# Optimization experiments

Hardware: AMD Instinct MI355X
Metric: run time of the kernel (lower is better)

The kernel has to match this reference:

```python
import jax, jax.numpy as jnp
import numpy as np

IN_FEATURES = 4096
OUT_FEATURES = 4096
NUM_TILES = 4


def setup_inputs() -> dict:
    key = jax.random.key(0)
    k1, k2, k3, k4 = jax.random.split(key, 4)
    x = jax.random.normal(k1, (4096, IN_FEATURES), dtype=jnp.float32)
    gate = jax.random.randint(k2, (4096, NUM_TILES), 0, 2, dtype=jnp.int32)
    # weights initialized ternary via sign(kaiming) in the module; emulate with sign(randn)
    weight = jnp.sign(jax.random.normal(k3, (OUT_FEATURES, IN_FEATURES), dtype=jnp.float32))
    scales = jax.random.uniform(k4, (OUT_FEATURES,), dtype=jnp.float32, minval=0.5, maxval=1.5)
    return {"x": x, "gate": gate, "weight": weight, "scales": scales}


def reference(x, gate, weight, scales):
    # TriX inference semantics: ternary (sign) weights, per-output scale,
    # per-sample tile gating of output columns.
    w = jnp.sign(weight)                       # [O, I] ternary
    out = jnp.matmul(x, w.T) * scales          # [B, O]
    tile_size = OUT_FEATURES // NUM_TILES
    # expand gate [B, T] -> mask over output features [B, O]
    mask = jnp.repeat(gate.astype(out.dtype), tile_size, axis=1)
    return out * mask
```

## Files before the change

kernel.cpp:

```cpp
#include <hip/hip_runtime.h>
#include <stdint.h>

#define M_DIM 4096
#define N_DIM 4096
#define K_DIM 4096
#define BM 128
#define BN 128
#define BKB 128

typedef __attribute__((ext_vector_type(4))) int     int4v;
typedef __attribute__((ext_vector_type(4))) float   f32x4;
typedef __attribute__((ext_vector_type(8))) uint8_t u8x8;

#define XSCALE (127.0f / 4.25f)
#define XDEQ   (4.25f / 127.0f)

__device__ __forceinline__ int8_t q8(float v) {
    float c = fminf(fmaxf(v * XSCALE, -127.0f), 127.0f);
    return (int8_t)(int)__builtin_rintf(c);
}
__device__ __forceinline__ int8_t s8(float v) {
    return (int8_t)((v > 0.0f) - (v < 0.0f));
}

__global__ __launch_bounds__(256) void cvt_i8_kernel(const float* __restrict__ x,
                                                     const float* __restrict__ w,
                                                     int8_t* __restrict__ xq,
                                                     int8_t* __restrict__ wq,
                                                     int n8each) {
    int idx = blockIdx.x * 256 + threadIdx.x;
    u8x8 o;
    if (idx < n8each) {
        const f32x4* s = (const f32x4*)x;
        f32x4 a = s[idx * 2], b = s[idx * 2 + 1];
        o[0] = (uint8_t)q8(a[0]); o[1] = (uint8_t)q8(a[1]);
        o[2] = (uint8_t)q8(a[2]); o[3] = (uint8_t)q8(a[3]);
        o[4] = (uint8_t)q8(b[0]); o[5] = (uint8_t)q8(b[1]);
        o[6] = (uint8_t)q8(b[2]); o[7] = (uint8_t)q8(b[3]);
        *(u8x8*)(xq + (size_t)idx * 8) = o;
    } else {
        int i = idx - n8each;
        const f32x4* s = (const f32x4*)w;
        f32x4 a = s[i * 2], b = s[i * 2 + 1];
        o[0] = (uint8_t)s8(a[0]); o[1] = (uint8_t)s8(a[1]);
        o[2] = (uint8_t)s8(a[2]); o[3] = (uint8_t)s8(a[3]);
        o[4] = (uint8_t)s8(b[0]); o[5] = (uint8_t)s8(b[1]);
        o[6] = (uint8_t)s8(b[2]); o[7] = (uint8_t)s8(b[3]);
        *(u8x8*)(wq + (size_t)i * 8) = o;
    }
}

__device__ __forceinline__ void gload_lds16(const int8_t* g, int8_t* l) {
    __builtin_amdgcn_global_load_lds(
        (__attribute__((address_space(1))) void*)(g),
        (__attribute__((address_space(3))) void*)(l),
        16, 0, 0);
}

__global__ __launch_bounds__(256, 2) void trix_gemm(
    const int8_t* __restrict__ A,
    const int8_t* __restrict__ B,
    const int* __restrict__ gate,
    const float* __restrict__ scales,
    float* __restrict__ out)
{
    __shared__ __align__(16) int8_t As[BM * BKB];
    __shared__ __align__(16) int8_t Bs[BN * BKB];

    const int tid  = threadIdx.x;
    const int lane = tid & 63;
    const int wave = tid >> 6;
    const int wm   = wave >> 1;
    const int wn   = wave & 1;
    const int quad = lane >> 4;
    const int ln16 = lane & 15;

    const int m0 = blockIdx.y * BM;
    const int n0 = blockIdx.x * BN;

    const int srow   = lane >> 3;
    const int gchunk = (lane & 7) ^ srow;
    const int8_t* a_src[4];
    const int8_t* b_src[4];
    int8_t* a_dst[4];
    int8_t* b_dst[4];
#pragma unroll
    for (int j = 0; j < 4; ++j) {
        int cidx = j * 4 + wave;
        a_src[j] = A + (size_t)(m0 + cidx * 8 + srow) * K_DIM + gchunk * 16;
        b_src[j] = B + (size_t)(n0 + cidx * 8 + srow) * K_DIM + gchunk * 16;
        a_dst[j] = As + cidx * 1024;
        b_dst[j] = Bs + cidx * 1024;
    }

    const int8_t* a_rd[4][2];
    const int8_t* b_rd[4][2];
#pragma unroll
    for (int i = 0; i < 4; ++i) {
        int arow = wm * 64 + i * 16 + ln16;
        int brow = wn * 64 + i * 16 + ln16;
#pragma unroll
        for (int kk = 0; kk < 2; ++kk) {
            int ch = quad + 4 * kk;
            a_rd[i][kk] = As + arow * 128 + ((ch ^ (arow & 7)) * 16);
            b_rd[i][kk] = Bs + brow * 128 + ((ch ^ (brow & 7)) * 16);
        }
    }

    int4v acc[4][4];
#pragma unroll
    for (int i = 0; i < 4; ++i)
#pragma unroll
        for (int j = 0; j < 4; ++j)
            acc[i][j] = (int4v){0, 0, 0, 0};

    for (int kt = 0; kt < K_DIM; kt += BKB) {
#pragma unroll
        for (int j = 0; j < 4; ++j) {
            gload_lds16(a_src[j], a_dst[j]);
            gload_lds16(b_src[j], b_dst[j]);
        }
#pragma unroll
        for (int j = 0; j < 4; ++j) { a_src[j] += BKB; b_src[j] += BKB; }
        __syncthreads();

#pragma unroll
        for (int kk = 0; kk < 2; ++kk) {
            int4v af[4], bf[4];
#pragma unroll
            for (int i = 0; i < 4; ++i) af[i] = *(const int4v*)a_rd[i][kk];
#pragma unroll
            for (int i = 0; i < 4; ++i) bf[i] = *(const int4v*)b_rd[i][kk];
#pragma unroll
            for (int i = 0; i < 4; ++i)
#pragma unroll
                for (int j = 0; j < 4; ++j)
                    acc[i][j] = __builtin_amdgcn_mfma_i32_16x16x64_i8(
                        af[i], bf[j], acc[i][j], 0, 0, 0);
        }
        __syncthreads();
    }

    const int gtile = n0 >> 10;
    float sc[4];
#pragma unroll
    for (int j = 0; j < 4; ++j) sc[j] = scales[n0 + wn * 64 + j * 16 + ln16] * XDEQ;

#pragma unroll
    for (int i = 0; i < 4; ++i) {
        int rbase = m0 + wm * 64 + i * 16 + quad * 4;
#pragma unroll
        for (int r = 0; r < 4; ++r) {
            int row = rbase + r;
            float g = (float)gate[row * 4 + gtile];
            float* orow = out + (size_t)row * N_DIM + n0 + wn * 64 + ln16;
#pragma unroll
            for (int j = 0; j < 4; ++j)
                orow[j * 16] = (float)acc[i][j][r] * sc[j] * g;
        }
    }
}

extern "C" void kernel_launch(void* const* d_in, const int* in_sizes, int n_in,
                              void* d_out, int out_size, void* d_ws, size_t ws_size,
                              hipStream_t stream) {
    const float* x      = (const float*)d_in[0];
    const int*   gate   = (const int*)d_in[1];
    const float* weight = (const float*)d_in[2];
    const float* scales = (const float*)d_in[3];
    float* out = (float*)d_out;

    int8_t* xq = (int8_t*)d_ws;
    int8_t* wq = xq + (size_t)M_DIM * K_DIM;

    const int n8each = M_DIM * K_DIM / 8;
    const int total_threads = 2 * n8each;
    cvt_i8_kernel<<<total_threads / 256, 256, 0, stream>>>(x, weight, xq, wq, n8each);

    dim3 grid(N_DIM / BN, M_DIM / BM);
    trix_gemm<<<grid, 256, 0, stream>>>(xq, wq, gate, scales, out);
}
```

Before: 230.4 us.

## Skip gated-off tiles by compacting active rows per tile and gathering

Builds per-tile lists of rows whose gate is set, using atomics inside the prep kernel, and zero-fills the output for gated-off row/tile pairs. The GEMM then runs over a 3D grid (column block, row block, tile), gathers the A rows through the index list, and exits early for row blocks past the active count. With random binary gates this avoids roughly half the int8 MFMA work. In exchange it adds a memset, atomics, an indirect row gather and scattered output stores.

After: 322.5 us. 40.0% more time.

```diff
diff --git a/kernel.cpp b/kernel.cpp
--- a/kernel.cpp
+++ b/kernel.cpp
@@ -8,9 +8,9 @@
 #define BN 128
 #define BKB 128
 
-typedef __attribute__((ext_vector_type(4))) int     int4v;
-typedef __attribute__((ext_vector_type(4))) float   f32x4;
-typedef __attribute__((ext_vector_type(8))) uint8_t u8x8;
+typedef __attribute__((ext_vector_type(4)))  int     int4v;
+typedef __attribute__((ext_vector_type(4)))  float   f32x4;
+typedef __attribute__((ext_vector_type(8)))  uint8_t u8x8;
 
 #define XSCALE (127.0f / 4.25f)
 #define XDEQ   (4.25f / 127.0f)
@@ -23,14 +23,16 @@
     return (int8_t)((v > 0.0f) - (v < 0.0f));
 }
 
-__global__ __launch_bounds__(256) void cvt_i8_kernel(const float* __restrict__ x,
-                                                     const float* __restrict__ w,
-                                                     int8_t* __restrict__ xq,
-                                                     int8_t* __restrict__ wq,
-                                                     int n8each) {
-    int idx = blockIdx.x * 256 + threadIdx.x;
+__global__ __launch_bounds__(256) void prep_kernel(
+    const float* __restrict__ x, const float* __restrict__ w,
+    const int* __restrict__ gate,
+    int8_t* __restrict__ xq, int8_t* __restrict__ wq,
+    float* __restrict__ out, int* __restrict__ list, int* __restrict__ cnt) {
+    const int bz  = blockIdx.x;
+    const int tid = threadIdx.x;
     u8x8 o;
-    if (idx < n8each) {
+    if (bz < 8192) {
+        int idx = bz * 256 + tid;
         const f32x4* s = (const f32x4*)x;
         f32x4 a = s[idx * 2], b = s[idx * 2 + 1];
         o[0] = (uint8_t)q8(a[0]); o[1] = (uint8_t)q8(a[1]);
@@ -38,15 +40,28 @@
         o[4] = (uint8_t)q8(b[0]); o[5] = (uint8_t)q8(b[1]);
         o[6] = (uint8_t)q8(b[2]); o[7] = (uint8_t)q8(b[3]);
         *(u8x8*)(xq + (size_t)idx * 8) = o;
-    } else {
-        int i = idx - n8each;
+    } else if (bz < 16384) {
+        int idx = (bz - 8192) * 256 + tid;
         const f32x4* s = (const f32x4*)w;
-        f32x4 a = s[i * 2], b = s[i * 2 + 1];
+        f32x4 a = s[idx * 2], b = s[idx * 2 + 1];
         o[0] = (uint8_t)s8(a[0]); o[1] = (uint8_t)s8(a[1]);
         o[2] = (uint8_t)s8(a[2]); o[3] = (uint8_t)s8(a[3]);
         o[4] = (uint8_t)s8(b[0]); o[5] = (uint8_t)s8(b[1]);
         o[6] = (uint8_t)s8(b[2]); o[7] = (uint8_t)s8(b[3]);
-        *(u8x8*)(wq + (size_t)i * 8) = o;
+        *(u8x8*)(wq + (size_t)idx * 8) = o;
+    } else if (bz < 32768) {
+        int z = bz - 16384;
+        int r = z >> 2, t = z & 3;
+        if (gate[r * 4 + t] != 0) return;
+        f32x4 zero = {0.f, 0.f, 0.f, 0.f};
+        *(f32x4*)(out + (size_t)r * N_DIM + t * 1024 + tid * 4) = zero;
+    } else {
+        int u = (bz - 32768) * 256 + tid;
+        int t = u >> 12, r = u & 4095;
+        if (gate[r * 4 + t] != 0) {
+            int pos = atomicAdd(&cnt[t], 1);
+            list[t * 4096 + pos] = r;
+        }
     }
 }
 
@@ -60,14 +75,27 @@
 __global__ __launch_bounds__(256, 2) void trix_gemm(
     const int8_t* __restrict__ A,
     const int8_t* __restrict__ B,
-    const int* __restrict__ gate,
+    const int* __restrict__ list,
+    const int* __restrict__ cnt,
     const float* __restrict__ scales,
     float* __restrict__ out)
 {
+    const int t     = blockIdx.z;
+    const int count = cnt[t];
+    const int rb    = blockIdx.y;
+    if (rb * 128 >= count) return;
+
     __shared__ __align__(16) int8_t As[BM * BKB];
     __shared__ __align__(16) int8_t Bs[BN * BKB];
+    __shared__ int ridx[128];
 
     const int tid  = threadIdx.x;
+    if (tid < 128) {
+        int i = rb * 128 + tid;
+        ridx[tid] = list[t * 4096 + min(i, count - 1)];
+    }
+    __syncthreads();
+
     const int lane = tid & 63;
     const int wave = tid >> 6;
     const int wm   = wave >> 1;
@@ -75,8 +103,7 @@
     const int quad = lane >> 4;
     const int ln16 = lane & 15;
 
-    const int m0 = blockIdx.y * BM;
-    const int n0 = blockIdx.x * BN;
+    const int n0 = t * 1024 + blockIdx.x * 128;
 
     const int srow   = lane >> 3;
     const int gchunk = (lane & 7) ^ srow;
@@ -87,7 +114,7 @@
 #pragma unroll
     for (int j = 0; j < 4; ++j) {
         int cidx = j * 4 + wave;
-        a_src[j] = A + (size_t)(m0 + cidx * 8 + srow) * K_DIM + gchunk * 16;
+        a_src[j] = A + (size_t)ridx[cidx * 8 + srow] * K_DIM + gchunk * 16;
         b_src[j] = B + (size_t)(n0 + cidx * 8 + srow) * K_DIM + gchunk * 16;
         a_dst[j] = As + cidx * 1024;
         b_dst[j] = Bs + cidx * 1024;
@@ -141,22 +168,20 @@
         __syncthreads();
     }
 
-    const int gtile = n0 >> 10;
     float sc[4];
 #pragma unroll
     for (int j = 0; j < 4; ++j) sc[j] = scales[n0 + wn * 64 + j * 16 + ln16] * XDEQ;
 
 #pragma unroll
     for (int i = 0; i < 4; ++i) {
-        int rbase = m0 + wm * 64 + i * 16 + quad * 4;
+        int lbase = wm * 64 + i * 16 + quad * 4;
 #pragma unroll
         for (int r = 0; r < 4; ++r) {
-            int row = rbase + r;
-            float g = (float)gate[row * 4 + gtile];
+            int row = ridx[lbase + r];
             float* orow = out + (size_t)row * N_DIM + n0 + wn * 64 + ln16;
 #pragma unroll
             for (int j = 0; j < 4; ++j)
-                orow[j * 16] = (float)acc[i][j][r] * sc[j] * g;
+                orow[j * 16] = (float)acc[i][j][r] * sc[j];
         }
     }
 }
@@ -170,13 +195,15 @@
     const float* scales = (const float*)d_in[3];
     float* out = (float*)d_out;
 
-    int8_t* xq = (int8_t*)d_ws;
-    int8_t* wq = xq + (size_t)M_DIM * K_DIM;
-
-    const int n8each = M_DIM * K_DIM / 8;
-    const int total_threads = 2 * n8each;
-    cvt_i8_kernel<<<total_threads / 256, 256, 0, stream>>>(x, weight, xq, wq, n8each);
-
-    dim3 grid(N_DIM / BN, M_DIM / BM);
-    trix_gemm<<<grid, 256, 0, stream>>>(xq, wq, gate, scales, out);
-}
+    int8_t* xq  = (int8_t*)d_ws;
+    int8_t* wq  = xq + (size_t)M_DIM * K_DIM;
+    int*    cnt = (int*)(wq + (size_t)M_DIM * K_DIM);
+    int*    list = cnt + 256;
+
+    hipMemsetAsync(cnt, 0, 16, stream);
+
+    prep_kernel<<<32832, 256, 0, stream>>>(x, weight, gate, xq, wq, out, list, cnt);
+
+    dim3 grid(8, 32, 4);
+    trix_gemm<<<grid, 256, 0, stream>>>(xq, wq, list, cnt, scales, out);
+}
```
